# Optimization experiments

Hardware: AMD Instinct MI355X
Metric: run time of the kernel (lower is better)

## Reference

```python
import jax, jax.numpy as jnp
import numpy as np

NTOKEN = 100000
NINP = 64
N_EDGES = 600000
BATCH = 64
MAX_LEN = 200


def gcn_conv(x, W, b, edge_index, num_nodes):
    # PyG GCNConv: add self-loops, symmetric normalization, x @ W then propagate.
    src, dst = edge_index[0], edge_index[1]
    loop = jnp.arange(num_nodes, dtype=src.dtype)
    src = jnp.concatenate([src, loop])
    dst = jnp.concatenate([dst, loop])
    deg = jax.ops.segment_sum(jnp.ones_like(dst, dtype=x.dtype), dst,
                              num_segments=num_nodes)
    dinv = jnp.where(deg > 0, deg ** -0.5, 0.0)
    norm = dinv[src] * dinv[dst]                      # [E+N]
    h = x @ W                                         # [N, out]
    out = jax.ops.segment_sum(h[src] * norm[:, None], dst,
                              num_segments=num_nodes)  # [N, out]
    return out + b


def setup_inputs() -> dict:
    key = jax.random.key(0)
    k_emb, k_w1, k_w2, k_e, k_in = jax.random.split(key, 5)
    # Xavier-normal scaled params
    emb = jax.random.normal(k_emb, (NTOKEN, NINP), jnp.float32) * (2.0 / (NTOKEN + NINP)) ** 0.5
    emb = emb.at[0].set(0.0)  # padding_idx=0
    W1 = jax.random.normal(k_w1, (NINP, 2 * NINP), jnp.float32) * (2.0 / (3 * NINP)) ** 0.5
    b1 = jnp.zeros((2 * NINP,), jnp.float32)
    W2 = jax.random.normal(k_w2, (2 * NINP, NINP), jnp.float32) * (2.0 / (3 * NINP)) ** 0.5
    b2 = jnp.zeros((NINP,), jnp.float32)
    edge_index = jax.random.randint(k_e, (2, N_EDGES), 0, NTOKEN, dtype=jnp.int32)
    inp = jax.random.randint(k_in, (BATCH, MAX_LEN), 0, NTOKEN, dtype=jnp.int32)
    return {"input": inp, "emb": emb, "W1": W1, "b1": b1,
            "W2": W2, "b2": b2, "edge_index": edge_index}


def reference(input, emb, W1, b1, W2, b2, edge_index):
    # GraphNN forward (eval mode: dropout = identity, no activation between convs)
    h = gcn_conv(emb, W1, b1, edge_index, NTOKEN)          # [N, 2*ninp]
    lookup = gcn_conv(h, W2, b2, edge_index, NTOKEN)       # [N, ninp]
    # one-hot scatter + einsum('bt,td->bd') is exactly a row gather:
    out = lookup[input]                                    # [B, L, ninp]
    return out
```

## Files before the change

### kernel.cpp

```cpp
#include <hip/hip_runtime.h>
#include <math.h>

static constexpr int NTOK = 100000;
static constexpr int NE   = 600000;
static constexpr int NPOS = 64 * 200;
static constexpr int CAP  = 32;
static constexpr int NBKT = 196;
static constexpr int BCAP = 5120;
static constexpr int EPB  = 2344;
static constexpr int EPT  = 10;

__global__ void k_setup(const float4* __restrict__ W14, const float* __restrict__ b1,
                        const float4* __restrict__ W24, float4* __restrict__ W124,
                        float4* __restrict__ bw4, int* __restrict__ bucketCnt) {
    int t = threadIdx.x;
    if (blockIdx.x < 4) {
        int j4 = t & 15;
        int k = blockIdx.x * 16 + (t >> 4);
        float4 acc = {0.f, 0.f, 0.f, 0.f};
        for (int mq = 0; mq < 32; ++mq) {
            float4 a = W14[k * 32 + mq];
            float4 w0 = W24[(4 * mq + 0) * 16 + j4];
            float4 w1 = W24[(4 * mq + 1) * 16 + j4];
            float4 w2 = W24[(4 * mq + 2) * 16 + j4];
            float4 w3 = W24[(4 * mq + 3) * 16 + j4];
            acc.x += a.x * w0.x + a.y * w1.x + a.z * w2.x + a.w * w3.x;
            acc.y += a.x * w0.y + a.y * w1.y + a.z * w2.y + a.w * w3.y;
            acc.z += a.x * w0.z + a.y * w1.z + a.z * w2.z + a.w * w3.z;
            acc.w += a.x * w0.w + a.y * w1.w + a.z * w2.w + a.w * w3.w;
        }
        W124[k * 16 + j4] = acc;
        if (blockIdx.x == 0 && t < 16) {
            float4 b = {0.f, 0.f, 0.f, 0.f};
            for (int m = 0; m < 128; ++m) {
                float a = b1[m];
                float4 w = W24[m * 16 + t];
                b.x += a * w.x; b.y += a * w.y; b.z += a * w.z; b.w += a * w.w;
            }
            bw4[t] = b;
        }
    } else {
        if (t < NBKT) bucketCnt[t] = 0;
    }
}

__global__ __launch_bounds__(256) void
k_bucket(const int* __restrict__ ei, int* __restrict__ bucketCnt,
         unsigned long long* __restrict__ buckets) {
    __shared__ int cnt[NBKT];
    __shared__ int base[NBKT];
    int t = threadIdx.x;
    if (t < NBKT) cnt[t] = 0;
    __syncthreads();

    int e0 = blockIdx.x * EPB;
    int eEnd = e0 + EPB; if (eEnd > NE) eEnd = NE;

    int s[EPT], d[EPT], r[EPT];
#pragma unroll
    for (int k = 0; k < EPT; ++k) {
        int i = e0 + t + k * 256;
        s[k] = -1; d[k] = 0; r[k] = 0;
        if (i < eEnd) {
            s[k] = ei[i];
            d[k] = ei[NE + i];
            r[k] = atomicAdd(&cnt[d[k] >> 9], 1);
        }
    }
    __syncthreads();
    if (t < NBKT) base[t] = atomicAdd(&bucketCnt[t], cnt[t]);
    __syncthreads();
#pragma unroll
    for (int k = 0; k < EPT; ++k) {
        if (s[k] >= 0) {
            int b = d[k] >> 9;
            int off = base[b] + r[k];
            if (off < BCAP)
                buckets[(long)b * BCAP + off] =
                    ((unsigned long long)(unsigned)s[k] << 32) | (unsigned)d[k];
        }
    }
}

__global__ __launch_bounds__(256) void
k_ellbuild(const unsigned long long* __restrict__ buckets,
           const int* __restrict__ bucketCnt, int* __restrict__ ell2,
           int* __restrict__ degs, float* __restrict__ dinv,
           float* __restrict__ dinv2) {
    __shared__ int cur[512];
    int t = threadIdx.x;
    cur[t] = 0; cur[t + 256] = 0;
    __syncthreads();

    int b = blockIdx.x;
    int n0 = b << 9;
    int m = bucketCnt[b]; if (m > BCAP) m = BCAP;
    const unsigned long long* bb = buckets + (long)b * BCAP;

    for (int i = t; i < m; i += 256) {
        unsigned long long v = bb[i];
        int dd = (int)(unsigned)v;
        int ss = (int)(v >> 32);
        int pos = atomicAdd(&cur[dd - n0], 1);
        if (pos < CAP) ell2[pos * NTOK + dd] = ss;
    }
    __syncthreads();
#pragma unroll
    for (int k = 0; k < 2; ++k) {
        int n = n0 + t + k * 256;
        if (n < NTOK) {
            int tot = cur[t + k * 256];
            degs[n] = tot < CAP ? tot : CAP;
            float dd = rsqrtf((float)tot + 1.0f);
            dinv[n] = dd;
            dinv2[n] = dd * dd;
        }
    }
}

__global__ void k_gatherA(const int* __restrict__ ell2, const int* __restrict__ degs,
                          const float* __restrict__ dinv, const float4* __restrict__ e4,
                          float4* __restrict__ u4, float* __restrict__ s_raw) {
    int idx = blockIdx.x * 256 + threadIdx.x;
    int n = idx >> 4;
    if (n >= NTOK) return;
    int jq = idx & 15;
    int d = degs[n];

    float cn = dinv[n];
    float4 v = e4[((long)n << 4) + jq];
    float4 s = {cn * v.x, cn * v.y, cn * v.z, cn * v.w};
    float sdv = cn;
    int e = 0;
    for (; e + 4 <= d; e += 4) {
        int s0 = ell2[(e + 0) * NTOK + n];
        int s1 = ell2[(e + 1) * NTOK + n];
        int s2 = ell2[(e + 2) * NTOK + n];
        int s3 = ell2[(e + 3) * NTOK + n];
        float c0 = dinv[s0], c1 = dinv[s1], c2 = dinv[s2], c3 = dinv[s3];
        float4 v0 = e4[((long)s0 << 4) + jq];
        float4 v1 = e4[((long)s1 << 4) + jq];
        float4 v2 = e4[((long)s2 << 4) + jq];
        float4 v3 = e4[((long)s3 << 4) + jq];
        s.x += c0 * v0.x + c1 * v1.x + c2 * v2.x + c3 * v3.x;
        s.y += c0 * v0.y + c1 * v1.y + c2 * v2.y + c3 * v3.y;
        s.z += c0 * v0.z + c1 * v1.z + c2 * v2.z + c3 * v3.z;
        s.w += c0 * v0.w + c1 * v1.w + c2 * v2.w + c3 * v3.w;
        sdv += (c0 + c1) + (c2 + c3);
    }
    for (; e < d; ++e) {
        int sx = ell2[e * NTOK + n];
        float c = dinv[sx];
        float4 v2 = e4[((long)sx << 4) + jq];
        s.x += c * v2.x; s.y += c * v2.y; s.z += c * v2.z; s.w += c * v2.w;
        sdv += c;
    }
    u4[((long)n << 4) + jq] = s;
    if (jq == 0) s_raw[n] = sdv;
}

__global__ __launch_bounds__(256) void
k_fused(const int* __restrict__ inp, const int* __restrict__ ell2,
        const int* __restrict__ degs, const float* __restrict__ dinv,
        const float* __restrict__ dinv2, const float* __restrict__ s_raw,
        const float* __restrict__ u, const float* __restrict__ W12,
        const float* __restrict__ bw, const float* __restrict__ b2,
        float* __restrict__ out) {
    __shared__ float w[64 * 64];
    int tid = threadIdx.x;
    {
        const float4* W4 = (const float4*)W12;
        float4* w4 = (float4*)w;
        for (int i = tid; i < 1024; i += 256) w4[i] = W4[i];
    }
    __syncthreads();

    int lane = tid & 63;
    int wid  = tid >> 6;
    int p = blockIdx.x * 4 + wid;
    int t = inp[p];
    int d = degs[t];

    float z = dinv2[t] * u[((long)t << 6) + lane];
    int e = 0;
    for (; e + 4 <= d; e += 4) {
        int s0 = ell2[(e + 0) * NTOK + t];
        int s1 = ell2[(e + 1) * NTOK + t];
        int s2 = ell2[(e + 2) * NTOK + t];
        int s3 = ell2[(e + 3) * NTOK + t];
        float c0 = dinv2[s0], c1 = dinv2[s1], c2 = dinv2[s2], c3 = dinv2[s3];
        float u0 = u[((long)s0 << 6) + lane];
        float u1 = u[((long)s1 << 6) + lane];
        float u2 = u[((long)s2 << 6) + lane];
        float u3 = u[((long)s3 << 6) + lane];
        z += (c0 * u0 + c1 * u1) + (c2 * u2 + c3 * u3);
    }
    for (; e < d; ++e) {
        int sx = ell2[e * NTOK + t];
        z += dinv2[sx] * u[((long)sx << 6) + lane];
    }
    z *= dinv[t];

    float o0 = 0.f, o1 = 0.f, o2 = 0.f, o3 = 0.f;
#pragma unroll
    for (int k = 0; k < 64; k += 4) {
        float z0 = __uint_as_float(__builtin_amdgcn_readlane(__float_as_uint(z), k));
        float z1 = __uint_as_float(__builtin_amdgcn_readlane(__float_as_uint(z), k + 1));
        float z2 = __uint_as_float(__builtin_amdgcn_readlane(__float_as_uint(z), k + 2));
        float z3 = __uint_as_float(__builtin_amdgcn_readlane(__float_as_uint(z), k + 3));
        o0 += z0 * w[(k + 0) * 64 + lane];
        o1 += z1 * w[(k + 1) * 64 + lane];
        o2 += z2 * w[(k + 2) * 64 + lane];
        o3 += z3 * w[(k + 3) * 64 + lane];
    }
    float o = (o0 + o1) + (o2 + o3) + dinv[t] * s_raw[t] * bw[lane] + b2[lane];
    out[((long)p << 6) + lane] = o;
}

extern "C" void kernel_launch(void* const* d_in, const int* in_sizes, int n_in,
                              void* d_out, int out_size, void* d_ws, size_t ws_size,
                              hipStream_t stream) {
    const int*   inp = (const int*)d_in[0];
    const float* emb = (const float*)d_in[1];
    const float* W1  = (const float*)d_in[2];
    const float* b1  = (const float*)d_in[3];
    const float* W2  = (const float*)d_in[4];
    const float* b2  = (const float*)d_in[5];
    const int*   ei  = (const int*)d_in[6];
    float* out = (float*)d_out;

    char* ws = (char*)d_ws;
    int*   bucketCnt = (int*)(ws + 0);
    float* W12   = (float*)(ws + 4096);
    float* bw    = (float*)(ws + 20480);
    int*   degs  = (int*)(ws + 24576);
    float* dinv  = (float*)(ws + 424576);
    float* dinv2 = (float*)(ws + 824576);
    float* s_raw = (float*)(ws + 1224576);
    unsigned long long* buckets = (unsigned long long*)(ws + 1624576);
    int*   ell2  = (int*)(ws + 9652736);
    float* u     = (float*)(ws + 22452736);

    k_setup<<<5, 256, 0, stream>>>((const float4*)W1, b1, (const float4*)W2,
                                   (float4*)W12, (float4*)bw, bucketCnt);

    k_bucket<<<256, 256, 0, stream>>>(ei, bucketCnt, buckets);

    k_ellbuild<<<NBKT, 256, 0, stream>>>(buckets, bucketCnt, ell2, degs, dinv, dinv2);

    int gblk = (NTOK * 16 + 255) / 256;
    k_gatherA<<<gblk, 256, 0, stream>>>(ell2, degs, dinv, (const float4*)emb,
                                        (float4*)u, s_raw);

    k_fused<<<NPOS / 4, 256, 0, stream>>>(inp, ell2, degs, dinv, dinv2,
                                          s_raw, u, W12, bw, b2, out);
}
```

Before: 83.82 us.

## Replace column-major ELL adjacency with bucketed CSR and coalesce bucket writes

Swaps the capped ELL layout (ell2[pos*NTOK+n]) for a per-bucket CSR built with a shared-memory counting sort, so each node's neighbours are contiguous and the CAP=32 truncation is gone. The bucketing kernel now stages edges in LDS sorted by bucket before writing them out, which makes the global stores contiguous instead of scattered. Gather kernels read neighbour lists from a contiguous row, cutting strided index loads. The cost is extra LDS prefix-scan passes and barriers in the build kernels.

```diff
diff --git a/kernel.cpp b/kernel.cpp
--- a/kernel.cpp
+++ b/kernel.cpp
@@ -4,11 +4,12 @@
 static constexpr int NTOK = 100000;
 static constexpr int NE   = 600000;
 static constexpr int NPOS = 64 * 200;
-static constexpr int CAP  = 32;
 static constexpr int NBKT = 196;
 static constexpr int BCAP = 5120;
 static constexpr int EPB  = 2344;
 static constexpr int EPT  = 10;
+
+typedef unsigned long long ull;
 
 __global__ void k_setup(const float4* __restrict__ W14, const float* __restrict__ b1,
                         const float4* __restrict__ W24, float4* __restrict__ W124,
@@ -40,85 +41,138 @@
             bw4[t] = b;
         }
     } else {
-        if (t < NBKT) bucketCnt[t] = 0;
+        bucketCnt[t] = 0;
     }
 }
 
 __global__ __launch_bounds__(256) void
 k_bucket(const int* __restrict__ ei, int* __restrict__ bucketCnt,
-         unsigned long long* __restrict__ buckets) {
-    __shared__ int cnt[NBKT];
-    __shared__ int base[NBKT];
+         ull* __restrict__ buckets) {
+    __shared__ int cnt[256];
+    __shared__ int pref[256];
+    __shared__ int eoff[256];
+    __shared__ int base[256];
+    __shared__ ull stg[EPB];
     int t = threadIdx.x;
-    if (t < NBKT) cnt[t] = 0;
+    cnt[t] = 0;
     __syncthreads();
 
     int e0 = blockIdx.x * EPB;
     int eEnd = e0 + EPB; if (eEnd > NE) eEnd = NE;
-
-    int s[EPT], d[EPT], r[EPT];
+    int tot = eEnd - e0;
+
+    int s_[EPT], d_[EPT], r_[EPT];
 #pragma unroll
     for (int k = 0; k < EPT; ++k) {
         int i = e0 + t + k * 256;
-        s[k] = -1; d[k] = 0; r[k] = 0;
+        s_[k] = -1;
         if (i < eEnd) {
-            s[k] = ei[i];
-            d[k] = ei[NE + i];
-            r[k] = atomicAdd(&cnt[d[k] >> 9], 1);
-        }
-    }
-    __syncthreads();
-    if (t < NBKT) base[t] = atomicAdd(&bucketCnt[t], cnt[t]);
-    __syncthreads();
+            s_[k] = ei[i];
+            d_[k] = ei[NE + i];
+            r_[k] = atomicAdd(&cnt[d_[k] >> 9], 1);
+        }
+    }
+    __syncthreads();
+
+    int v = cnt[t];
+    pref[t] = v;
+    __syncthreads();
+    for (int o = 1; o < 256; o <<= 1) {
+        int x = pref[t];
+        if (t >= o) x += pref[t - o];
+        __syncthreads();
+        pref[t] = x;
+        __syncthreads();
+    }
+    eoff[t] = pref[t] - v;
+    base[t] = (v > 0) ? atomicAdd(&bucketCnt[t], v) : 0;
+    __syncthreads();
+
 #pragma unroll
     for (int k = 0; k < EPT; ++k) {
-        if (s[k] >= 0) {
-            int b = d[k] >> 9;
-            int off = base[b] + r[k];
-            if (off < BCAP)
-                buckets[(long)b * BCAP + off] =
-                    ((unsigned long long)(unsigned)s[k] << 32) | (unsigned)d[k];
-        }
+        if (s_[k] >= 0) {
+            int b = d_[k] >> 9;
+            stg[eoff[b] + r_[k]] =
+                ((ull)(unsigned)s_[k] << 32) | (unsigned)d_[k];
+        }
+    }
+    __syncthreads();
+
+    for (int i = t; i < tot; i += 256) {
+        ull e = stg[i];
+        int b = ((int)(unsigned)e) >> 9;
+        int off = base[b] + (i - eoff[b]);
+        if (off < BCAP) buckets[(long)b * BCAP + off] = e;
     }
 }
 
 __global__ __launch_bounds__(256) void
-k_ellbuild(const unsigned long long* __restrict__ buckets,
-           const int* __restrict__ bucketCnt, int* __restrict__ ell2,
-           int* __restrict__ degs, float* __restrict__ dinv,
-           float* __restrict__ dinv2) {
+k_csrbuild(const ull* __restrict__ buckets, const int* __restrict__ bucketCnt,
+           int* __restrict__ csr, int* __restrict__ roff, int* __restrict__ degs,
+           float* __restrict__ dinv, float* __restrict__ dinv2) {
+    __shared__ int cnt[512];
+    __shared__ int pref[512];
     __shared__ int cur[512];
+    __shared__ int bsum[256];
+    __shared__ int stg[BCAP];
     int t = threadIdx.x;
-    cur[t] = 0; cur[t + 256] = 0;
+    cnt[t] = 0; cnt[t + 256] = 0;
     __syncthreads();
 
     int b = blockIdx.x;
     int n0 = b << 9;
     int m = bucketCnt[b]; if (m > BCAP) m = BCAP;
-    const unsigned long long* bb = buckets + (long)b * BCAP;
+    const ull* bb = buckets + (long)b * BCAP;
 
     for (int i = t; i < m; i += 256) {
-        unsigned long long v = bb[i];
+        int dd = (int)(unsigned)bb[i];
+        atomicAdd(&cnt[dd - n0], 1);
+    }
+    __syncthreads();
+
+    int a0 = cnt[2 * t], a1 = cnt[2 * t + 1];
+    bsum[t] = a0 + a1;
+    __syncthreads();
+    for (int o = 1; o < 256; o <<= 1) {
+        int x = bsum[t];
+        if (t >= o) x += bsum[t - o];
+        __syncthreads();
+        bsum[t] = x;
+        __syncthreads();
+    }
+    int eb = bsum[t] - (a0 + a1);
+    pref[2 * t] = eb;       cur[2 * t] = eb;
+    pref[2 * t + 1] = eb + a0; cur[2 * t + 1] = eb + a0;
+    __syncthreads();
+
+    for (int i = t; i < m; i += 256) {
+        ull v = bb[i];
         int dd = (int)(unsigned)v;
         int ss = (int)(v >> 32);
         int pos = atomicAdd(&cur[dd - n0], 1);
-        if (pos < CAP) ell2[pos * NTOK + dd] = ss;
-    }
-    __syncthreads();
+        stg[pos] = ss;
+    }
+    __syncthreads();
+
+    for (int i = t; i < m; i += 256) csr[(long)b * BCAP + i] = stg[i];
+
 #pragma unroll
     for (int k = 0; k < 2; ++k) {
-        int n = n0 + t + k * 256;
+        int l = t + k * 256;
+        int n = n0 + l;
         if (n < NTOK) {
-            int tot = cur[t + k * 256];
-            degs[n] = tot < CAP ? tot : CAP;
-            float dd = rsqrtf((float)tot + 1.0f);
+            int dg = cnt[l];
+            degs[n] = dg;
+            roff[n] = b * BCAP + pref[l];
+            float dd = rsqrtf((float)dg + 1.0f);
             dinv[n] = dd;
             dinv2[n] = dd * dd;
         }
     }
 }
 
-__global__ void k_gatherA(const int* __restrict__ ell2, const int* __restrict__ degs,
+__global__ void k_gatherA(const int* __restrict__ csr, const int* __restrict__ roff,
+                          const int* __restrict__ degs,
                           const float* __restrict__ dinv, const float4* __restrict__ e4,
                           float4* __restrict__ u4, float* __restrict__ s_raw) {
     int idx = blockIdx.x * 256 + threadIdx.x;
@@ -126,6 +180,7 @@
     if (n >= NTOK) return;
     int jq = idx & 15;
     int d = degs[n];
+    const int* row = csr + roff[n];
 
     float cn = dinv[n];
     float4 v = e4[((long)n << 4) + jq];
@@ -133,10 +188,7 @@
     float sdv = cn;
     int e = 0;
     for (; e + 4 <= d; e += 4) {
-        int s0 = ell2[(e + 0) * NTOK + n];
-        int s1 = ell2[(e + 1) * NTOK + n];
-        int s2 = ell2[(e + 2) * NTOK + n];
-        int s3 = ell2[(e + 3) * NTOK + n];
+        int s0 = row[e], s1 = row[e + 1], s2 = row[e + 2], s3 = row[e + 3];
         float c0 = dinv[s0], c1 = dinv[s1], c2 = dinv[s2], c3 = dinv[s3];
         float4 v0 = e4[((long)s0 << 4) + jq];
         float4 v1 = e4[((long)s1 << 4) + jq];
@@ -149,7 +201,7 @@
         sdv += (c0 + c1) + (c2 + c3);
     }
     for (; e < d; ++e) {
-        int sx = ell2[e * NTOK + n];
+        int sx = row[e];
         float c = dinv[sx];
         float4 v2 = e4[((long)sx << 4) + jq];
         s.x += c * v2.x; s.y += c * v2.y; s.z += c * v2.z; s.w += c * v2.w;
@@ -160,12 +212,12 @@
 }
 
 __global__ __launch_bounds__(256) void
-k_fused(const int* __restrict__ inp, const int* __restrict__ ell2,
-        const int* __restrict__ degs, const float* __restrict__ dinv,
-        const float* __restrict__ dinv2, const float* __restrict__ s_raw,
-        const float* __restrict__ u, const float* __restrict__ W12,
-        const float* __restrict__ bw, const float* __restrict__ b2,
-        float* __restrict__ out) {
+k_fused(const int* __restrict__ inp, const int* __restrict__ csr,
+        const int* __restrict__ roff, const int* __restrict__ degs,
+        const float* __restrict__ dinv, const float* __restrict__ dinv2,
+        const float* __restrict__ s_raw, const float* __restrict__ u,
+        const float* __restrict__ W12, const float* __restrict__ bw,
+        const float* __restrict__ b2, float* __restrict__ out) {
     __shared__ float w[64 * 64];
     int tid = threadIdx.x;
     {
@@ -180,14 +232,12 @@
     int p = blockIdx.x * 4 + wid;
     int t = inp[p];
     int d = degs[t];
+    const int* row = csr + roff[t];
 
     float z = dinv2[t] * u[((long)t << 6) + lane];
     int e = 0;
     for (; e + 4 <= d; e += 4) {
-        int s0 = ell2[(e + 0) * NTOK + t];
-        int s1 = ell2[(e + 1) * NTOK + t];
-        int s2 = ell2[(e + 2) * NTOK + t];
-        int s3 = ell2[(e + 3) * NTOK + t];
+        int s0 = row[e], s1 = row[e + 1], s2 = row[e + 2], s3 = row[e + 3];
         float c0 = dinv2[s0], c1 = dinv2[s1], c2 = dinv2[s2], c3 = dinv2[s3];
         float u0 = u[((long)s0 << 6) + lane];
         float u1 = u[((long)s1 << 6) + lane];
@@ -196,7 +246,7 @@
         z += (c0 * u0 + c1 * u1) + (c2 * u2 + c3 * u3);
     }
     for (; e < d; ++e) {
-        int sx = ell2[e * NTOK + t];
+        int sx = row[e];
         z += dinv2[sx] * u[((long)sx << 6) + lane];
     }
     z *= dinv[t];
@@ -237,21 +287,23 @@
     float* dinv  = (float*)(ws + 424576);
     float* dinv2 = (float*)(ws + 824576);
     float* s_raw = (float*)(ws + 1224576);
-    unsigned long long* buckets = (unsigned long long*)(ws + 1624576);
-    int*   ell2  = (int*)(ws + 9652736);
-    float* u     = (float*)(ws + 22452736);
+    int*   roff  = (int*)(ws + 1624576);
+    ull*   buckets = (ull*)(ws + 2024576);
+    int*   csr   = (int*)(ws + 10052736);
+    float* u     = (float*)(ws + 14066816);
 
     k_setup<<<5, 256, 0, stream>>>((const float4*)W1, b1, (const float4*)W2,
                                    (float4*)W12, (float4*)bw, bucketCnt);
 
     k_bucket<<<256, 256, 0, stream>>>(ei, bucketCnt, buckets);
 
-    k_ellbuild<<<NBKT, 256, 0, stream>>>(buckets, bucketCnt, ell2, degs, dinv, dinv2);
+    k_csrbuild<<<NBKT, 256, 0, stream>>>(buckets, bucketCnt, csr, roff,
+                                         degs, dinv, dinv2);
 
     int gblk = (NTOK * 16 + 255) / 256;
-    k_gatherA<<<gblk, 256, 0, stream>>>(ell2, degs, dinv, (const float4*)emb,
+    k_gatherA<<<gblk, 256, 0, stream>>>(csr, roff, degs, dinv, (const float4*)emb,
                                         (float4*)u, s_raw);
 
-    k_fused<<<NPOS / 4, 256, 0, stream>>>(inp, ell2, degs, dinv, dinv2,
+    k_fused<<<NPOS / 4, 256, 0, stream>>>(inp, csr, roff, degs, dinv, dinv2,
                                           s_raw, u, W12, bw, b2, out);
 }
```

Result: no change. 83.63 us (-0.2%).
